# Optimization experiments

Hardware: AMD Instinct MI355X
Metric: run time of the kernel (lower is better)

## Reference

```python
import jax, jax.numpy as jnp
import numpy as np

V, E, P, T = 65536, 4096, 4096, 512
SENT = 1e9    # finite sentinel for masked min/max (keeps grads NaN-free)
BIG = 1e30    # 'never the minimum' sentinel for invalid points


def setup_inputs() -> dict:
    key = jax.random.key(0)
    k1, k2, k3, k4 = jax.random.split(key, 4)
    verts = jax.random.uniform(k1, (V, 3), dtype=jnp.float32)
    e0 = jax.random.randint(k2, (E,), 0, V - 1)
    edges = jnp.stack([e0, e0 + 1], axis=1)          # distinct endpoints
    listAll = jax.random.randint(k3, (P,), 0, V)
    TableR = jax.random.uniform(k4, (T, 7), dtype=jnp.float32)
    return {"verts": verts, "TableR": TableR, "edges": edges,
            "listAll": listAll, "epoch": 1, "pth": 0}


def _mouth_loss(verts, TableR, edges, listAll):
    v2 = verts[:, :2]                 # deleteaxeZ
    p = v2[listAll]                   # [P,2] query points
    px, py = p[:, 0], p[:, 1]
    ev = v2[edges]                    # [E,2,2]
    x0, y0 = ev[:, 0, 0], ev[:, 0, 1]
    x1, y1 = ev[:, 1, 0], ev[:, 1, 1]
    a = (y0 - y1) / (x0 - x1)         # edge line y = a*x + b (order-invariant)
    b = y0 - a * x0

    # getexpose: first edge with min_x < px < max_x (falls back to last edge)
    xmn, xmx = jnp.minimum(x0, x1), jnp.maximum(x0, x1)
    condA = (px[:, None] > xmn[None, :]) & (px[:, None] < xmx[None, :])  # [P,E]
    idx = jnp.where(condA.any(1), jnp.argmax(condA, axis=1), E - 1)
    exposeY = a[idx] * px + b[idx]
    L1 = jnp.sqrt((py - exposeY) ** 2)        # expose shares x with p -> dx=0
    cy = (py + exposeY) * 0.5                 # centre1 = midpoint (cx == px)
    cx = px

    # getpoints: intersections of horizontal ray y=cy with every edge
    ymn, ymx = jnp.minimum(y0, y1), jnp.maximum(y0, y1)
    condB = (cy[:, None] > ymn[None, :]) & (cy[:, None] < ymx[None, :])  # [P,E]
    xi = (cy[:, None] - b[None, :]) / a[None, :]                          # [P,E]
    n = condB.sum(1)
    xall_mx = jnp.max(jnp.where(condB, xi, -SENT), axis=1)
    xall_mn = jnp.min(jnp.where(condB, xi, SENT), axis=1)
    spu = condB & (xi >= cx[:, None])   # right side (incl. equal, per original)
    inf_ = condB & (xi < cx[:, None])   # left side
    xs = jnp.min(jnp.where(spu, xi, SENT), axis=1)    # minimum of spu
    xinf = jnp.max(jnp.where(inf_, xi, -SENT), axis=1)  # maximum of inf
    has_both = spu.any(1) & inf_.any(1)
    valid = (n == 2) | ((n > 2) & has_both)
    dx = jnp.where(n == 2, xall_mx - xall_mn, xs - xinf)
    L2 = jnp.sqrt(dx ** 2)                    # both points share y=cy
    d1 = jnp.sqrt((cy - 1.0) ** 2)            # dist([1, cy], Ref=(1,1))
    d2 = jnp.sqrt((px - 1.0) ** 2)            # dist([px, 1], Ref=(1,1))

    # al vs every table row (only columns 3..6 are used by the original)
    al = (jnp.abs(L1[:, None] - TableR[None, :, 3])
          + jnp.abs(L2[:, None] - TableR[None, :, 4])
          + jnp.abs(d1[:, None] - TableR[None, :, 5])
          + jnp.abs(d2[:, None] - TableR[None, :, 6]))          # [P,T]
    pm = jnp.min(al, axis=1)                  # per-point best table match
    # `error` is never reset in the original -> running min across points
    m = jnp.where(valid, pm, BIG)
    run = jax.lax.cummin(m, axis=0)
    return jnp.sum(jnp.where(valid, run, 0.0))


def reference(verts, TableR, edges, listAll, epoch, pth):
    # epoch/pth only gate .obj file dumping in the original; no math effect.
    return _mouth_loss(verts, TableR, edges, listAll)
```

## Files before the change

kernel.cpp:

```cpp
#include <hip/hip_runtime.h>
#include <math.h>

#define NV 65536
#define NE 4096
#define NP 4096
#define NT 512
#define SENTF 1000000000.0f
#define BIGF 1e30f

__device__ __forceinline__ float waveMinF(float v) {
    #pragma unroll
    for (int o = 32; o; o >>= 1) v = fminf(v, __shfl_xor(v, o, 64));
    return v;
}
__device__ __forceinline__ float waveMaxF(float v) {
    #pragma unroll
    for (int o = 32; o; o >>= 1) v = fmaxf(v, __shfl_xor(v, o, 64));
    return v;
}
__device__ __forceinline__ int waveSumI(int v) {
    #pragma unroll
    for (int o = 32; o; o >>= 1) v += __shfl_xor(v, o, 64);
    return v;
}
__device__ __forceinline__ int waveMinI(int v) {
    #pragma unroll
    for (int o = 32; o; o >>= 1) v = min(v, __shfl_xor(v, o, 64));
    return v;
}

__global__ void prep_kernel(const float* __restrict__ verts,
                            const int*   __restrict__ edges,
                            const float* __restrict__ tab,
                            float*  __restrict__ ea,  float*  __restrict__ eb,
                            float2* __restrict__ pk2, float4* __restrict__ pk4,
                            float4* __restrict__ tb4) {
    int e = blockIdx.x * blockDim.x + threadIdx.x;
    if (e < NT) {
        const float* r = tab + 7 * e;
        tb4[e] = make_float4(r[3], r[4], r[5], r[6]);
    }
    if (e >= NE) return;
    int i0 = edges[2 * e + 0];
    int i1 = edges[2 * e + 1];
    float x0 = verts[3 * i0 + 0], y0 = verts[3 * i0 + 1];
    float x1 = verts[3 * i1 + 0], y1 = verts[3 * i1 + 1];
    float a = (y0 - y1) / (x0 - x1);
    float b = y0 - a * x0;
    ea[e] = a; eb[e] = b;
    pk2[e] = make_float2(fminf(x0, x1), fmaxf(x0, x1));
    pk4[e] = make_float4(fminf(y0, y1), fmaxf(y0, y1), 1.0f / a, b);
}

__global__ __launch_bounds__(256) void point_kernel(
        const float*  __restrict__ verts,
        const int*    __restrict__ listAll,
        const float*  __restrict__ ea,  const float*  __restrict__ eb,
        const float2* __restrict__ pk2, const float4* __restrict__ pk4,
        const float4* __restrict__ tb4,
        float* __restrict__ mOut, int* __restrict__ vOut) {
    __shared__ float sCY[4], sPX[4], sL1[4], sL2[4];
    __shared__ float sQ[4][4][6];
    __shared__ float sF[4][6];
    __shared__ int   sVal[4];

    const int tid  = threadIdx.x;
    const int lane = tid & 63;
    const int w    = tid >> 6;
    const int pBase = blockIdx.x * 4;

    {
        int p  = pBase + w;
        int vi = listAll[p];
        float px = verts[3 * vi + 0];
        float py = verts[3 * vi + 1];
        int minIdx = NE;
        for (int it = 0; it < NE / 64; ++it) {
            int e = it * 64 + lane;
            float2 q = pk2[e];
            bool hit = (px > q.x) && (px < q.y);
            if (hit) minIdx = e;
            if (__any(hit)) break;
        }
        minIdx = waveMinI(minIdx);
        int idx = (minIdx >= NE) ? (NE - 1) : minIdx;
        float exposeY = ea[idx] * px + eb[idx];
        if (lane == 0) {
            sCY[w] = 0.5f * (py + exposeY);
            sL1[w] = fabsf(py - exposeY);
            sPX[w] = px;
        }
    }
    __syncthreads();

    float cyv[4], cxv[4];
    #pragma unroll
    for (int p = 0; p < 4; ++p) { cyv[p] = sCY[p]; cxv[p] = sPX[p]; }

    float mx[4], mn[4], xs[4], xf[4];
    int   nC[4], hh[4];
    #pragma unroll
    for (int p = 0; p < 4; ++p) {
        mx[p] = -SENTF; mn[p] = SENTF; xs[p] = SENTF; xf[p] = -SENTF;
        nC[p] = 0; hh[p] = 0;
    }

    #pragma unroll 4
    for (int it = 0; it < 16; ++it) {
        float4 q = pk4[w * 1024 + it * 64 + lane];
        #pragma unroll
        for (int p = 0; p < 4; ++p) {
            float cy = cyv[p], cx = cxv[p];
            bool  c  = (cy > q.x) && (cy < q.y);
            float xi = (cy - q.w) * q.z;
            nC[p] += c ? 1 : 0;
            mx[p] = fmaxf(mx[p], c ? xi : -SENTF);
            mn[p] = fminf(mn[p], c ? xi :  SENTF);
            bool sp  = c && (xi >= cx);
            bool in_ = c && (xi <  cx);
            xs[p] = fminf(xs[p], sp  ? xi :  SENTF);
            xf[p] = fmaxf(xf[p], in_ ? xi : -SENTF);
            hh[p] |= (sp ? 1 : 0) | (in_ ? 0x10000 : 0);
        }
    }

    #pragma unroll
    for (int p = 0; p < 4; ++p) {
        float a0 = waveMaxF(mx[p]);
        float a1 = waveMinF(mn[p]);
        float a2 = waveMinF(xs[p]);
        float a3 = waveMaxF(xf[p]);
        int   a4 = waveSumI(nC[p]);
        int   a5 = waveSumI(hh[p]);
        if (lane == 0) {
            sQ[w][p][0] = a0; sQ[w][p][1] = a1;
            sQ[w][p][2] = a2; sQ[w][p][3] = a3;
            sQ[w][p][4] = __int_as_float(a4);
            sQ[w][p][5] = __int_as_float(a5);
        }
    }
    __syncthreads();

    if (tid < 24) {
        int p = tid & 3, s = tid >> 2;
        if (s == 0)      sF[p][0] = fmaxf(fmaxf(sQ[0][p][0], sQ[1][p][0]), fmaxf(sQ[2][p][0], sQ[3][p][0]));
        else if (s == 1) sF[p][1] = fminf(fminf(sQ[0][p][1], sQ[1][p][1]), fminf(sQ[2][p][1], sQ[3][p][1]));
        else if (s == 2) sF[p][2] = fminf(fminf(sQ[0][p][2], sQ[1][p][2]), fminf(sQ[2][p][2], sQ[3][p][2]));
        else if (s == 3) sF[p][3] = fmaxf(fmaxf(sQ[0][p][3], sQ[1][p][3]), fmaxf(sQ[2][p][3], sQ[3][p][3]));
        else if (s == 4) sF[p][4] = __int_as_float(__float_as_int(sQ[0][p][4]) + __float_as_int(sQ[1][p][4])
                                                 + __float_as_int(sQ[2][p][4]) + __float_as_int(sQ[3][p][4]));
        else             sF[p][5] = __int_as_float(__float_as_int(sQ[0][p][5]) + __float_as_int(sQ[1][p][5])
                                                 + __float_as_int(sQ[2][p][5]) + __float_as_int(sQ[3][p][5]));
    }
    __syncthreads();

    if (tid < 4) {
        int n  = __float_as_int(sF[tid][4]);
        int hc = __float_as_int(sF[tid][5]);
        int hS = hc & 0xFFFF, hI = hc >> 16;
        bool valid = (n == 2) || ((n > 2) && (hS > 0) && (hI > 0));
        float dx = (n == 2) ? (sF[tid][0] - sF[tid][1]) : (sF[tid][2] - sF[tid][3]);
        sL2[tid]  = fabsf(dx);
        sVal[tid] = valid ? 1 : 0;
    }
    __syncthreads();

    {
        float L1v = sL1[w], L2v = sL2[w];
        float d1  = fabsf(sCY[w] - 1.0f);
        float d2  = fabsf(sPX[w] - 1.0f);
        float pm = INFINITY;
        #pragma unroll
        for (int kk = 0; kk < NT / 64; ++kk) {
            float4 r = tb4[kk * 64 + lane];
            float al = fabsf(L1v - r.x) + fabsf(L2v - r.y) +
                       fabsf(d1 - r.z) + fabsf(d2 - r.w);
            pm = fminf(pm, al);
        }
        pm = waveMinF(pm);
        if (lane == 0) {
            mOut[pBase + w] = sVal[w] ? pm : BIGF;
            vOut[pBase + w] = sVal[w];
        }
    }
}

__global__ __launch_bounds__(1024) void scan_kernel(const float* __restrict__ m,
                                                    const int*   __restrict__ valid,
                                                    float* __restrict__ out) {
    __shared__ float wAgg[16];
    __shared__ float wSum[16];
    int t = threadIdx.x;
    int lane = t & 63, wid = t >> 6;

    float v[4]; int vl[4];
    #pragma unroll
    for (int j = 0; j < 4; j++) { v[j] = m[4 * t + j]; vl[j] = valid[4 * t + j]; }
    float cmin = fminf(fminf(v[0], v[1]), fminf(v[2], v[3]));

    float inc = cmin;
    #pragma unroll
    for (int o = 1; o < 64; o <<= 1) {
        float u = __shfl_up(inc, o, 64);
        if (lane >= o) inc = fminf(inc, u);
    }
    if (lane == 63) wAgg[wid] = inc;
    __syncthreads();

    float wavePrefix = INFINITY;
    for (int i = 0; i < wid; i++) wavePrefix = fminf(wavePrefix, wAgg[i]);
    float excl = __shfl_up(inc, 1, 64);
    if (lane == 0) excl = INFINITY;
    float run = fminf(wavePrefix, excl);

    float sum = 0.0f;
    #pragma unroll
    for (int j = 0; j < 4; j++) {
        run = fminf(run, v[j]);
        if (vl[j]) sum += run;
    }
    #pragma unroll
    for (int o = 32; o; o >>= 1) sum += __shfl_xor(sum, o, 64);
    if (lane == 0) wSum[wid] = sum;
    __syncthreads();
    if (t == 0) {
        float s = 0.0f;
        for (int i = 0; i < 16; i++) s += wSum[i];
        out[0] = s;
    }
}

extern "C" void kernel_launch(void* const* d_in, const int* in_sizes, int n_in,
                              void* d_out, int out_size, void* d_ws, size_t ws_size,
                              hipStream_t stream) {
    const float* verts   = (const float*)d_in[0];
    const float* tab     = (const float*)d_in[1];
    const int*   edges   = (const int*)d_in[2];
    const int*   listAll = (const int*)d_in[3];

    char* ws = (char*)d_ws;
    float4* pk4 = (float4*)ws;                    ws += NE * sizeof(float4);
    float4* tb4 = (float4*)ws;                    ws += NT * sizeof(float4);
    float2* pk2 = (float2*)ws;                    ws += NE * sizeof(float2);
    float*  ea  = (float*)ws;                     ws += NE * sizeof(float);
    float*  eb  = (float*)ws;                     ws += NE * sizeof(float);
    float*  mArr= (float*)ws;                     ws += NP * sizeof(float);
    int*    vArr= (int*)ws;

    prep_kernel<<<(NE + 255) / 256, 256, 0, stream>>>(verts, edges, tab,
                                                      ea, eb, pk2, pk4, tb4);
    point_kernel<<<NP / 4, 256, 0, stream>>>(verts, listAll,
                                             ea, eb, pk2, pk4, tb4,
                                             mArr, vArr);
    scan_kernel<<<1, 1024, 0, stream>>>(mArr, vArr, (float*)d_out);
}
```

Measured before the change: 27.50 us.

## Split point kernel into expose-search and ray-intersection kernels with unrolled search

```diff
diff --git a/kernel.cpp b/kernel.cpp
--- a/kernel.cpp
+++ b/kernel.cpp
@@ -32,8 +32,8 @@
 __global__ void prep_kernel(const float* __restrict__ verts,
                             const int*   __restrict__ edges,
                             const float* __restrict__ tab,
-                            float*  __restrict__ ea,  float*  __restrict__ eb,
-                            float2* __restrict__ pk2, float4* __restrict__ pk4,
+                            float*  __restrict__ ea,   float*  __restrict__ eb,
+                            float4* __restrict__ pk14, float4* __restrict__ pk4,
                             float4* __restrict__ tb4) {
     int e = blockIdx.x * blockDim.x + threadIdx.x;
     if (e < NT) {
@@ -48,20 +48,67 @@
     float a = (y0 - y1) / (x0 - x1);
     float b = y0 - a * x0;
     ea[e] = a; eb[e] = b;
-    pk2[e] = make_float2(fminf(x0, x1), fmaxf(x0, x1));
-    pk4[e] = make_float4(fminf(y0, y1), fmaxf(y0, y1), 1.0f / a, b);
-}
-
-__global__ __launch_bounds__(256) void point_kernel(
+    pk14[e] = make_float4(fminf(x0, x1), fmaxf(x0, x1), a, b);
+    pk4[e]  = make_float4(fminf(y0, y1), fmaxf(y0, y1), 1.0f / a, b);
+}
+
+__global__ __launch_bounds__(256) void pointA_kernel(
         const float*  __restrict__ verts,
         const int*    __restrict__ listAll,
-        const float*  __restrict__ ea,  const float*  __restrict__ eb,
-        const float2* __restrict__ pk2, const float4* __restrict__ pk4,
-        const float4* __restrict__ tb4,
+        const float*  __restrict__ ea, const float* __restrict__ eb,
+        const float4* __restrict__ pk14,
+        float* __restrict__ cyArr, float* __restrict__ l1Arr,
+        float* __restrict__ pxArr) {
+    const int lane = threadIdx.x & 63;
+    const int w    = threadIdx.x >> 6;
+    const int p    = blockIdx.x * 4 + w;
+
+    int   vi = listAll[p];
+    float px = verts[3 * vi + 0];
+    float py = verts[3 * vi + 1];
+
+    int   idxSel = NE;
+    float aSel = 0.f, bSel = 0.f;
+    for (int it = 0; it < NE / 256; ++it) {
+        int e0 = it * 256 + lane;
+        float4 qa = pk14[e0];
+        float4 qb = pk14[e0 + 64];
+        float4 qc = pk14[e0 + 128];
+        float4 qd = pk14[e0 + 192];
+        bool h0 = (px > qa.x) && (px < qa.y);
+        bool h1 = (px > qb.x) && (px < qb.y);
+        bool h2 = (px > qc.x) && (px < qc.y);
+        bool h3 = (px > qd.x) && (px < qd.y);
+        int il = NE; float as = 0.f, bs = 0.f;
+        if (h3) { il = e0 + 192; as = qd.z; bs = qd.w; }
+        if (h2) { il = e0 + 128; as = qc.z; bs = qc.w; }
+        if (h1) { il = e0 + 64;  as = qb.z; bs = qb.w; }
+        if (h0) { il = e0;       as = qa.z; bs = qa.w; }
+        bool any4 = h0 | h1 | h2 | h3;
+        if (any4) { idxSel = il; aSel = as; bSel = bs; }
+        if (__any(any4)) break;
+    }
+    int mi = waveMinI(idxSel);
+    float a_ = __shfl(aSel, mi & 63, 64);
+    float b_ = __shfl(bSel, mi & 63, 64);
+    if (mi >= NE) { a_ = ea[NE - 1]; b_ = eb[NE - 1]; }
+
+    float exposeY = a_ * px + b_;
+    if (lane == 0) {
+        cyArr[p] = 0.5f * (py + exposeY);
+        l1Arr[p] = fabsf(py - exposeY);
+        pxArr[p] = px;
+    }
+}
+
+__global__ __launch_bounds__(256) void pointB_kernel(
+        const float4* __restrict__ pk4,  const float4* __restrict__ tb4,
+        const float*  __restrict__ cyArr, const float* __restrict__ l1Arr,
+        const float*  __restrict__ pxArr,
         float* __restrict__ mOut, int* __restrict__ vOut) {
-    __shared__ float sCY[4], sPX[4], sL1[4], sL2[4];
     __shared__ float sQ[4][4][6];
     __shared__ float sF[4][6];
+    __shared__ float sL2[4];
     __shared__ int   sVal[4];
 
     const int tid  = threadIdx.x;
@@ -69,33 +116,12 @@
     const int w    = tid >> 6;
     const int pBase = blockIdx.x * 4;
 
-    {
-        int p  = pBase + w;
-        int vi = listAll[p];
-        float px = verts[3 * vi + 0];
-        float py = verts[3 * vi + 1];
-        int minIdx = NE;
-        for (int it = 0; it < NE / 64; ++it) {
-            int e = it * 64 + lane;
-            float2 q = pk2[e];
-            bool hit = (px > q.x) && (px < q.y);
-            if (hit) minIdx = e;
-            if (__any(hit)) break;
-        }
-        minIdx = waveMinI(minIdx);
-        int idx = (minIdx >= NE) ? (NE - 1) : minIdx;
-        float exposeY = ea[idx] * px + eb[idx];
-        if (lane == 0) {
-            sCY[w] = 0.5f * (py + exposeY);
-            sL1[w] = fabsf(py - exposeY);
-            sPX[w] = px;
-        }
-    }
-    __syncthreads();
-
     float cyv[4], cxv[4];
     #pragma unroll
-    for (int p = 0; p < 4; ++p) { cyv[p] = sCY[p]; cxv[p] = sPX[p]; }
+    for (int p = 0; p < 4; ++p) {
+        cyv[p] = cyArr[pBase + p];
+        cxv[p] = pxArr[pBase + p];
+    }
 
     float mx[4], mn[4], xs[4], xf[4];
     int   nC[4], hh[4];
@@ -166,9 +192,9 @@
     __syncthreads();
 
     {
-        float L1v = sL1[w], L2v = sL2[w];
-        float d1  = fabsf(sCY[w] - 1.0f);
-        float d2  = fabsf(sPX[w] - 1.0f);
+        float L1v = l1Arr[pBase + w], L2v = sL2[w];
+        float d1  = fabsf(cyv[w] - 1.0f);
+        float d2  = fabsf(cxv[w] - 1.0f);
         float pm = INFINITY;
         #pragma unroll
         for (int kk = 0; kk < NT / 64; ++kk) {
@@ -239,18 +265,22 @@
     const int*   listAll = (const int*)d_in[3];
 
     char* ws = (char*)d_ws;
-    float4* pk4 = (float4*)ws;                    ws += NE * sizeof(float4);
-    float4* tb4 = (float4*)ws;                    ws += NT * sizeof(float4);
-    float2* pk2 = (float2*)ws;                    ws += NE * sizeof(float2);
-    float*  ea  = (float*)ws;                     ws += NE * sizeof(float);
-    float*  eb  = (float*)ws;                     ws += NE * sizeof(float);
-    float*  mArr= (float*)ws;                     ws += NP * sizeof(float);
-    int*    vArr= (int*)ws;
+    float4* pk4  = (float4*)ws;                   ws += NE * sizeof(float4);
+    float4* pk14 = (float4*)ws;                   ws += NE * sizeof(float4);
+    float4* tb4  = (float4*)ws;                   ws += NT * sizeof(float4);
+    float*  ea   = (float*)ws;                    ws += NE * sizeof(float);
+    float*  eb   = (float*)ws;                    ws += NE * sizeof(float);
+    float*  cyArr= (float*)ws;                    ws += NP * sizeof(float);
+    float*  l1Arr= (float*)ws;                    ws += NP * sizeof(float);
+    float*  pxArr= (float*)ws;                    ws += NP * sizeof(float);
+    float*  mArr = (float*)ws;                    ws += NP * sizeof(float);
+    int*    vArr = (int*)ws;
 
     prep_kernel<<<(NE + 255) / 256, 256, 0, stream>>>(verts, edges, tab,
-                                                      ea, eb, pk2, pk4, tb4);
-    point_kernel<<<NP / 4, 256, 0, stream>>>(verts, listAll,
-                                             ea, eb, pk2, pk4, tb4,
-                                             mArr, vArr);
+                                                      ea, eb, pk14, pk4, tb4);
+    pointA_kernel<<<NP / 4, 256, 0, stream>>>(verts, listAll, ea, eb, pk14,
+                                              cyArr, l1Arr, pxArr);
+    pointB_kernel<<<NP / 4, 256, 0, stream>>>(pk4, tb4, cyArr, l1Arr, pxArr,
+                                              mArr, vArr);
     scan_kernel<<<1, 1024, 0, stream>>>(mArr, vArr, (float*)d_out);
 }
```

Result: slower. 30.25 us (+10.0%).
